# Performance work log

Hardware: AMD Instinct MI355X
Metric: run time of the kernel (lower is better)

## Reference

```python
import jax, jax.numpy as jnp
import numpy as np

B, S, D, K = 8, 1024, 1024, 8192


def setup_inputs() -> dict:
    key = jax.random.key(0)
    k1, k2 = jax.random.split(key)
    z = jax.random.normal(k1, (B, S, D), dtype=jnp.float32)
    codebook = jax.random.normal(k2, (K, D), dtype=jnp.float32)
    return {"z": z, "codebook": codebook}


def reference(z, codebook):
    # Eval-mode forward of VectorQuantizer (no EMA / dead-code side effects).
    b, s, d = z.shape
    z_flat = z.reshape(-1, d)                              # [N, D]
    # squared L2 distances: ||z||^2 + ||e||^2 - 2 z.e
    distances = (jnp.sum(z_flat * z_flat, axis=1, keepdims=True)
                 + jnp.sum(codebook * codebook, axis=1)
                 - 2.0 * jnp.einsum('nd,kd->nk', z_flat, codebook))  # [N, K]
    indices = jnp.argmin(distances, axis=1)                # [N]
    quantized = codebook[indices].reshape(b, s, d)         # gather
    loss = jnp.asarray(0.0, dtype=z.dtype)                 # eval mode
    # straight-through estimator
    quantized = z + jax.lax.stop_gradient(quantized - z)
    logits = -distances.reshape(b, s, -1)                  # [B, S, K]
    return quantized, indices.reshape(b, s), loss, logits
```

## Files before the change

kernel.cpp:

```cpp
#include <hip/hip_runtime.h>
#include <hip/hip_bf16.h>
#include <stdint.h>

#define NROWS 8192
#define KCODES 8192
#define DDIM 1024

#define Q_OFF    0
#define IDX_OFF  8388608
#define LOSS_OFF 8396800
#define LOG_OFF  8396801

using f32x4  = __attribute__((ext_vector_type(4))) float;
using s16x8  = __attribute__((ext_vector_type(8))) short;

__device__ __forceinline__ unsigned int forder(float f) {
  unsigned int u = __float_as_uint(f);
  return (u & 0x80000000u) ? ~u : (u | 0x80000000u);
}
__device__ __forceinline__ float finv(unsigned int u) {
  return (u & 0x80000000u) ? __uint_as_float(u & 0x7fffffffu) : __uint_as_float(~u);
}

__device__ __forceinline__ void gld_lds16(const void* g, void* l) {
  __builtin_amdgcn_global_load_lds((const __attribute__((address_space(1))) unsigned int*)g,
                                   (__attribute__((address_space(3))) unsigned int*)l,
                                   16, 0, 0);
}

__global__ __launch_bounds__(256) void vq_convert(const float* __restrict__ z,
                                                  const float* __restrict__ cb,
                                                  __hip_bfloat16* __restrict__ bfbuf,
                                                  float* __restrict__ nrm) {
  const int r = blockIdx.x;
  const float* src = (r < NROWS) ? (z + (size_t)r * DDIM)
                                 : (cb + (size_t)(r - NROWS) * DDIM);
  float4 v = reinterpret_cast<const float4*>(src)[threadIdx.x];
  float vv[4] = {v.x, v.y, v.z, v.w};
  ushort4 p;
  unsigned short us[4];
  #pragma unroll
  for (int j = 0; j < 4; ++j) {
    __hip_bfloat16 b = __float2bfloat16(vv[j]);
    __builtin_memcpy(&us[j], &b, 2);
  }
  p.x = us[0]; p.y = us[1]; p.z = us[2]; p.w = us[3];
  reinterpret_cast<ushort4*>(bfbuf + (size_t)r * DDIM)[threadIdx.x] = p;

  float s = vv[0]*vv[0] + vv[1]*vv[1] + vv[2]*vv[2] + vv[3]*vv[3];
  #pragma unroll
  for (int m = 32; m > 0; m >>= 1) s += __shfl_down(s, m, 64);
  __shared__ float red[4];
  if ((threadIdx.x & 63) == 0) red[threadIdx.x >> 6] = s;
  __syncthreads();
  if (threadIdx.x == 0) nrm[r] = red[0] + red[1] + red[2] + red[3];
}

__global__ __launch_bounds__(256, 3) void vq_mfma(const __hip_bfloat16* __restrict__ zb,
                                                  const __hip_bfloat16* __restrict__ cbb,
                                                  const float* __restrict__ nrm,
                                                  unsigned int* __restrict__ gmins,
                                                  float* __restrict__ out) {
  __shared__ s16x8 Asv[1024];
  __shared__ s16x8 Bsv[1024];

  const int wgid = blockIdx.x;
  const int stx = wgid & 7;
  const int idx = wgid >> 3;
  const int sty = idx >> 6;
  const int tt_ = idx & 63;
  const int bx = stx * 8 + (tt_ & 7);
  const int by = sty * 8 + (tt_ >> 3);

  const int k0 = bx * 128;
  const int n0 = by * 128;
  const int tid = threadIdx.x;
  const int wid = tid >> 6, lane = tid & 63;
  const int wm = wid >> 1, wn = wid & 1;
  const int l15 = lane & 15, l4 = lane >> 4;

  const int srow = lane >> 3;
  const int c    = lane & 7;
  const __hip_bfloat16* ga[4];
  const __hip_bfloat16* gb[4];
  int loff[4];
  #pragma unroll
  for (int q = 0; q < 4; ++q) {
    const int s = wid * 4 + q;
    const int row = s * 8 + srow;
    const int cg = c ^ (row & 7);
    ga[q] = zb  + (size_t)(n0 + row) * DDIM + cg * 8;
    gb[q] = cbb + (size_t)(k0 + row) * DDIM + cg * 8;
    loff[q] = s * 1024;
  }

  f32x4 acc[4][4];
  #pragma unroll
  for (int i = 0; i < 4; ++i)
    #pragma unroll
    for (int j = 0; j < 4; ++j) acc[i][j] = (f32x4){0.f, 0.f, 0.f, 0.f};

  for (int it = 0; it < 16; ++it) {
    const int d0 = it * 64;
    #pragma unroll
    for (int q = 0; q < 4; ++q) {
      gld_lds16(ga[q] + d0, (char*)Asv + loff[q]);
      gld_lds16(gb[q] + d0, (char*)Bsv + loff[q]);
    }
    __syncthreads();

    #pragma unroll
    for (int ks = 0; ks < 2; ++ks) {
      const int ch = ks * 4 + l4;
      s16x8 af[4], bf[4];
      #pragma unroll
      for (int f = 0; f < 4; ++f) {
        const int ar = wm * 64 + f * 16 + l15;
        af[f] = Asv[ar * 8 + (ch ^ (ar & 7))];
        const int br = wn * 64 + f * 16 + l15;
        bf[f] = Bsv[br * 8 + (ch ^ (br & 7))];
      }
      #pragma unroll
      for (int fm = 0; fm < 4; ++fm)
        #pragma unroll
        for (int fn = 0; fn < 4; ++fn)
          acc[fm][fn] = __builtin_amdgcn_mfma_f32_16x16x32_bf16(af[fm], bf[fn], acc[fm][fn], 0, 0, 0);
    }
    __syncthreads();
  }

  float ee[4];
  #pragma unroll
  for (int j = 0; j < 4; ++j) ee[j] = nrm[NROWS + k0 + wn * 64 + j * 16 + l15];

  float* logits = out + LOG_OFF;
  #pragma unroll
  for (int f = 0; f < 4; ++f) {
    #pragma unroll
    for (int r = 0; r < 4; ++r) {
      const int n = n0 + wm * 64 + f * 16 + l4 * 4 + r;
      const float zz = nrm[n];
      float rowmin = 3.4e38f;
      #pragma unroll
      for (int j = 0; j < 4; ++j) {
        const int k = k0 + wn * 64 + j * 16 + l15;
        const float dist = fmaf(-2.f, acc[f][j][r], zz + ee[j]);
        logits[(size_t)n * KCODES + k] = -dist;
        rowmin = fminf(rowmin, dist);
      }
      #pragma unroll
      for (int mm = 1; mm < 16; mm <<= 1)
        rowmin = fminf(rowmin, __shfl_xor(rowmin, mm, 64));
      if (l15 == 0) atomicMin(&gmins[(size_t)n * 32 + (bx >> 1)], forder(rowmin));
    }
  }
}

#define MARGIN 16.0f
__global__ __launch_bounds__(256) void vq_refine(const float* __restrict__ z,
                                                 const float* __restrict__ cb,
                                                 const float* __restrict__ nrm,
                                                 const unsigned int* __restrict__ gmins,
                                                 float* __restrict__ out) {
  const int n = blockIdx.x;
  const int tid = threadIdx.x;
  __shared__ float tminS[32];
  __shared__ float gminS;
  __shared__ int cnt;
  __shared__ int cand[64];
  __shared__ float red[4];

  if (tid < 32) tminS[tid] = finv(gmins[(size_t)n * 32 + tid]);
  if (tid == 0) cnt = 0;
  __syncthreads();
  if (tid == 0) {
    float g = tminS[0];
    #pragma unroll
    for (int i = 1; i < 32; ++i) g = fminf(g, tminS[i]);
    gminS = g;
  }
  __syncthreads();
  const float thr = gminS + MARGIN;

  const float* lrow = out + LOG_OFF + (size_t)n * KCODES;
  for (int g = 0; g < 32; ++g) {
    if (tminS[g] <= thr) {
      const float dist = -lrow[g * 256 + tid];
      if (dist <= thr) {
        const int p = atomicAdd(&cnt, 1);
        if (p < 64) cand[p] = g * 256 + tid;
      }
    }
  }
  __syncthreads();
  const int ncand = min(cnt, 64);

  const float zz = nrm[n];
  const float4 zv = reinterpret_cast<const float4*>(z + (size_t)n * DDIM)[tid];
  float bestd = 0.f;
  int bestk = -1;
  for (int ci = 0; ci < ncand; ++ci) {
    const int k = cand[ci];
    const float4 ev = reinterpret_cast<const float4*>(cb + (size_t)k * DDIM)[tid];
    float s = zv.x * ev.x + zv.y * ev.y + zv.z * ev.z + zv.w * ev.w;
    #pragma unroll
    for (int mm = 32; mm > 0; mm >>= 1) s += __shfl_down(s, mm, 64);
    if ((tid & 63) == 0) red[tid >> 6] = s;
    __syncthreads();
    const float dot = red[0] + red[1] + red[2] + red[3];
    const float dist = zz + nrm[NROWS + k] - 2.0f * dot;
    if (bestk < 0 || dist < bestd || (dist == bestd && k < bestk)) {
      bestd = dist; bestk = k;
    }
    __syncthreads();
  }

  const float4* src = reinterpret_cast<const float4*>(cb + (size_t)bestk * DDIM);
  float4* dst = reinterpret_cast<float4*>(out + (size_t)n * DDIM);
  dst[tid] = src[tid];
  if (tid == 0) {
    out[IDX_OFF + n] = (float)bestk;
    if (n == 0) out[LOSS_OFF] = 0.f;
  }
}

extern "C" void kernel_launch(void* const* d_in, const int* in_sizes, int n_in,
                              void* d_out, int out_size, void* d_ws, size_t ws_size,
                              hipStream_t stream) {
  const float* z  = (const float*)d_in[0];
  const float* cb = (const float*)d_in[1];
  float* out = (float*)d_out;

  float* nrm = (float*)d_ws;
  unsigned int* gmins = (unsigned int*)((char*)d_ws + 65536);

  __hip_bfloat16* bfbuf = (__hip_bfloat16*)out;
  const __hip_bfloat16* zbf  = bfbuf;
  const __hip_bfloat16* cbbf = bfbuf + (size_t)NROWS * DDIM;

  hipMemsetAsync((char*)d_ws + 65536, 0xFF, (size_t)NROWS * 32 * 4, stream);
  vq_convert<<<NROWS + KCODES, 256, 0, stream>>>(z, cb, bfbuf, nrm);
  vq_mfma<<<4096, 256, 0, stream>>>(zbf, cbbf, nrm, gmins, out);
  vq_refine<<<NROWS, 256, 0, stream>>>(z, cb, nrm, gmins, out);
}
```

Before: 231.4 us.

## Stage logits tile through LDS for aligned vectorized nontemporal stores

The logits region starts at an odd float offset, so scalar per-element stores are misaligned. The epilogue now writes each 128x128 distance tile into a swizzled LDS buffer shifted by one column. It then emits 16-byte-aligned nontemporal vector stores, with a few boundary columns written as scalars. It also hoists the row-norm loads and raises the launch-bounds occupancy hint from 3 to 4, which may add register pressure and extra barriers in the epilogue.

```diff
diff --git a/kernel.cpp b/kernel.cpp
--- a/kernel.cpp
+++ b/kernel.cpp
@@ -56,13 +56,14 @@
   if (threadIdx.x == 0) nrm[r] = red[0] + red[1] + red[2] + red[3];
 }
 
-__global__ __launch_bounds__(256, 3) void vq_mfma(const __hip_bfloat16* __restrict__ zb,
+__global__ __launch_bounds__(256, 4) void vq_mfma(const __hip_bfloat16* __restrict__ zb,
                                                   const __hip_bfloat16* __restrict__ cbb,
                                                   const float* __restrict__ nrm,
                                                   unsigned int* __restrict__ gmins,
                                                   float* __restrict__ out) {
-  __shared__ s16x8 Asv[1024];
-  __shared__ s16x8 Bsv[1024];
+  __shared__ s16x8 smem[2048];
+  s16x8* Asv = smem;
+  s16x8* Bsv = smem + 1024;
 
   const int wgid = blockIdx.x;
   const int stx = wgid & 7;
@@ -132,26 +133,71 @@
   float ee[4];
   #pragma unroll
   for (int j = 0; j < 4; ++j) ee[j] = nrm[NROWS + k0 + wn * 64 + j * 16 + l15];
+  float zzv[4][4];
+  #pragma unroll
+  for (int f = 0; f < 4; ++f)
+    #pragma unroll
+    for (int r = 0; r < 4; ++r)
+      zzv[f][r] = nrm[n0 + wm * 64 + f * 16 + l4 * 4 + r];
 
   float* logits = out + LOG_OFF;
+
   #pragma unroll
   for (int f = 0; f < 4; ++f) {
     #pragma unroll
     for (int r = 0; r < 4; ++r) {
       const int n = n0 + wm * 64 + f * 16 + l4 * 4 + r;
-      const float zz = nrm[n];
       float rowmin = 3.4e38f;
       #pragma unroll
       for (int j = 0; j < 4; ++j) {
-        const int k = k0 + wn * 64 + j * 16 + l15;
-        const float dist = fmaf(-2.f, acc[f][j][r], zz + ee[j]);
-        logits[(size_t)n * KCODES + k] = -dist;
+        const int col = wn * 64 + j * 16 + l15;
+        const float dist = fmaf(-2.f, acc[f][j][r], zzv[f][r] + ee[j]);
+        if ((j == 0 && wn == 0 && l15 < 3) || (j == 3 && wn == 1 && l15 == 15))
+          logits[(size_t)n * KCODES + k0 + col] = -dist;
         rowmin = fminf(rowmin, dist);
       }
       #pragma unroll
       for (int mm = 1; mm < 16; mm <<= 1)
         rowmin = fminf(rowmin, __shfl_xor(rowmin, mm, 64));
       if (l15 == 0) atomicMin(&gmins[(size_t)n * 32 + (bx >> 1)], forder(rowmin));
+    }
+  }
+
+  float* tb = (float*)smem;
+  #pragma unroll 1
+  for (int p = 0; p < 2; ++p) {
+    __syncthreads();
+    if (wm == p) {
+      #pragma unroll
+      for (int f = 0; f < 4; ++f) {
+        const int rowl_base = f * 16 + l4 * 4;
+        #pragma unroll
+        for (int r = 0; r < 4; ++r) {
+          const int rowl = rowl_base + r;
+          #pragma unroll
+          for (int j = 0; j < 4; ++j) {
+            const int col = wn * 64 + j * 16 + l15;
+            if (col < 127) {
+              const float dist = fmaf(-2.f, acc[f][j][r], zzv[f][r] + ee[j]);
+              const int cs = col + 1;
+              tb[rowl * 128 + (((cs >> 2) ^ (rowl & 31)) << 2) + (cs & 3)] = -dist;
+            }
+          }
+        }
+      }
+    }
+    __syncthreads();
+    const int row = tid & 63;
+    const int cg = tid >> 6;
+    const int n = n0 + p * 64 + row;
+    float* lb = out + (LOG_OFF - 1) + (size_t)n * KCODES + k0;
+    #pragma unroll
+    for (int m = 0; m < 8; ++m) {
+      const int cc = cg * 8 + m;
+      if (cc >= 1) {
+        f32x4 v = *reinterpret_cast<f32x4*>(tb + row * 128 + ((cc ^ (row & 31)) << 2));
+        __builtin_nontemporal_store(v, reinterpret_cast<f32x4*>(lb + 4 * cc));
+      }
     }
   }
 }
```

New measurement: 731.0 us. +215.9%, slower.

## Switch distance GEMM from bf16 to per-row scaled int8 MFMA

Applied to the files above, without the earlier changes.

Quantizes z and codebook rows to int8 with per-row absmax scales in the convert kernel and uses the i8 16x16x64 MFMA instruction, halving the K-loop iterations and the bytes staged through LDS. The epilogue rescales the int32 accumulators by both row scales to rebuild the fp32 distances. Occupancy hint is raised to 4 blocks per CU. This trades accuracy of the approximate logits for higher matrix throughput, and relies on the fp32 refine pass and its margin to recover exact argmin indices; the written logits become coarser approximations of the reference values.

```diff
diff --git a/kernel.cpp b/kernel.cpp
--- a/kernel.cpp
+++ b/kernel.cpp
@@ -12,7 +12,7 @@
 #define LOG_OFF  8396801
 
 using f32x4  = __attribute__((ext_vector_type(4))) float;
-using s16x8  = __attribute__((ext_vector_type(8))) short;
+using i32x4  = __attribute__((ext_vector_type(4))) int;
 
 __device__ __forceinline__ unsigned int forder(float f) {
   unsigned int u = __float_as_uint(f);
@@ -30,39 +30,55 @@
 
 __global__ __launch_bounds__(256) void vq_convert(const float* __restrict__ z,
                                                   const float* __restrict__ cb,
-                                                  __hip_bfloat16* __restrict__ bfbuf,
-                                                  float* __restrict__ nrm) {
+                                                  signed char* __restrict__ qbuf,
+                                                  float* __restrict__ nrm,
+                                                  float* __restrict__ scl) {
   const int r = blockIdx.x;
+  const int tid = threadIdx.x;
   const float* src = (r < NROWS) ? (z + (size_t)r * DDIM)
                                  : (cb + (size_t)(r - NROWS) * DDIM);
-  float4 v = reinterpret_cast<const float4*>(src)[threadIdx.x];
+  float4 v = reinterpret_cast<const float4*>(src)[tid];
   float vv[4] = {v.x, v.y, v.z, v.w};
-  ushort4 p;
-  unsigned short us[4];
+
+  float amax = fmaxf(fmaxf(fabsf(vv[0]), fabsf(vv[1])),
+                     fmaxf(fabsf(vv[2]), fabsf(vv[3])));
+  float ss = vv[0]*vv[0] + vv[1]*vv[1] + vv[2]*vv[2] + vv[3]*vv[3];
+  #pragma unroll
+  for (int m = 32; m > 0; m >>= 1) {
+    amax = fmaxf(amax, __shfl_down(amax, m, 64));
+    ss += __shfl_down(ss, m, 64);
+  }
+  __shared__ float rA[4], rS[4], sB;
+  if ((tid & 63) == 0) { rA[tid >> 6] = amax; rS[tid >> 6] = ss; }
+  __syncthreads();
+  if (tid == 0) {
+    const float a = fmaxf(fmaxf(rA[0], rA[1]), fmaxf(rA[2], rA[3]));
+    nrm[r] = rS[0] + rS[1] + rS[2] + rS[3];
+    const float s = fmaxf(a, 1e-20f) * (1.0f / 127.0f);
+    scl[r] = s;
+    sB = s;
+  }
+  __syncthreads();
+  const float inv = 1.0f / sB;
+  int q[4];
   #pragma unroll
   for (int j = 0; j < 4; ++j) {
-    __hip_bfloat16 b = __float2bfloat16(vv[j]);
-    __builtin_memcpy(&us[j], &b, 2);
-  }
-  p.x = us[0]; p.y = us[1]; p.z = us[2]; p.w = us[3];
-  reinterpret_cast<ushort4*>(bfbuf + (size_t)r * DDIM)[threadIdx.x] = p;
-
-  float s = vv[0]*vv[0] + vv[1]*vv[1] + vv[2]*vv[2] + vv[3]*vv[3];
-  #pragma unroll
-  for (int m = 32; m > 0; m >>= 1) s += __shfl_down(s, m, 64);
-  __shared__ float red[4];
-  if ((threadIdx.x & 63) == 0) red[threadIdx.x >> 6] = s;
-  __syncthreads();
-  if (threadIdx.x == 0) nrm[r] = red[0] + red[1] + red[2] + red[3];
-}
-
-__global__ __launch_bounds__(256, 3) void vq_mfma(const __hip_bfloat16* __restrict__ zb,
-                                                  const __hip_bfloat16* __restrict__ cbb,
+    int t = (int)rintf(vv[j] * inv);
+    q[j] = t < -127 ? -127 : (t > 127 ? 127 : t);
+  }
+  const int packed = (q[0] & 255) | ((q[1] & 255) << 8) |
+                     ((q[2] & 255) << 16) | (q[3] << 24);
+  reinterpret_cast<int*>(qbuf + (size_t)r * DDIM)[tid] = packed;
+}
+
+__global__ __launch_bounds__(256, 4) void vq_mfma(const signed char* __restrict__ zq,
+                                                  const signed char* __restrict__ cq,
                                                   const float* __restrict__ nrm,
+                                                  const float* __restrict__ scl,
                                                   unsigned int* __restrict__ gmins,
                                                   float* __restrict__ out) {
-  __shared__ s16x8 Asv[1024];
-  __shared__ s16x8 Bsv[1024];
+  __shared__ i32x4 Asv[1024];
+  __shared__ i32x4 Bsv[1024];
 
   const int wgid = blockIdx.x;
   const int stx = wgid & 7;
@@ -81,27 +97,27 @@
 
   const int srow = lane >> 3;
   const int c    = lane & 7;
-  const __hip_bfloat16* ga[4];
-  const __hip_bfloat16* gb[4];
+  const signed char* ga[4];
+  const signed char* gb[4];
   int loff[4];
   #pragma unroll
   for (int q = 0; q < 4; ++q) {
     const int s = wid * 4 + q;
     const int row = s * 8 + srow;
     const int cg = c ^ (row & 7);
-    ga[q] = zb  + (size_t)(n0 + row) * DDIM + cg * 8;
-    gb[q] = cbb + (size_t)(k0 + row) * DDIM + cg * 8;
+    ga[q] = zq + (size_t)(n0 + row) * DDIM + cg * 16;
+    gb[q] = cq + (size_t)(k0 + row) * DDIM + cg * 16;
     loff[q] = s * 1024;
   }
 
-  f32x4 acc[4][4];
+  i32x4 acc[4][4];
   #pragma unroll
   for (int i = 0; i < 4; ++i)
     #pragma unroll
-    for (int j = 0; j < 4; ++j) acc[i][j] = (f32x4){0.f, 0.f, 0.f, 0.f};
-
-  for (int it = 0; it < 16; ++it) {
-    const int d0 = it * 64;
+    for (int j = 0; j < 4; ++j) acc[i][j] = (i32x4){0, 0, 0, 0};
+
+  for (int it = 0; it < 8; ++it) {
+    const int d0 = it * 128;
     #pragma unroll
     for (int q = 0; q < 4; ++q) {
       gld_lds16(ga[q] + d0, (char*)Asv + loff[q]);
@@ -112,7 +128,7 @@
     #pragma unroll
     for (int ks = 0; ks < 2; ++ks) {
       const int ch = ks * 4 + l4;
-      s16x8 af[4], bf[4];
+      i32x4 af[4], bf[4];
       #pragma unroll
       for (int f = 0; f < 4; ++f) {
         const int ar = wm * 64 + f * 16 + l15;
@@ -124,14 +140,18 @@
       for (int fm = 0; fm < 4; ++fm)
         #pragma unroll
         for (int fn = 0; fn < 4; ++fn)
-          acc[fm][fn] = __builtin_amdgcn_mfma_f32_16x16x32_bf16(af[fm], bf[fn], acc[fm][fn], 0, 0, 0);
-    }
-    __syncthreads();
-  }
-
-  float ee[4];
-  #pragma unroll
-  for (int j = 0; j < 4; ++j) ee[j] = nrm[NROWS + k0 + wn * 64 + j * 16 + l15];
+          acc[fm][fn] = __builtin_amdgcn_mfma_i32_16x16x64_i8(af[fm], bf[fn], acc[fm][fn], 0, 0, 0);
+    }
+    __syncthreads();
+  }
+
+  float ee[4], sk[4];
+  #pragma unroll
+  for (int j = 0; j < 4; ++j) {
+    const int kk = k0 + wn * 64 + j * 16 + l15;
+    ee[j] = nrm[NROWS + kk];
+    sk[j] = scl[NROWS + kk];
+  }
 
   float* logits = out + LOG_OFF;
   #pragma unroll
@@ -140,11 +160,12 @@
     for (int r = 0; r < 4; ++r) {
       const int n = n0 + wm * 64 + f * 16 + l4 * 4 + r;
       const float zz = nrm[n];
+      const float sn2 = -2.0f * scl[n];
       float rowmin = 3.4e38f;
       #pragma unroll
       for (int j = 0; j < 4; ++j) {
         const int k = k0 + wn * 64 + j * 16 + l15;
-        const float dist = fmaf(-2.f, acc[f][j][r], zz + ee[j]);
+        const float dist = fmaf(sn2 * sk[j], (float)acc[f][j][r], zz + ee[j]);
         logits[(size_t)n * KCODES + k] = -dist;
         rowmin = fminf(rowmin, dist);
       }
@@ -232,14 +253,15 @@
   float* out = (float*)d_out;
 
   float* nrm = (float*)d_ws;
-  unsigned int* gmins = (unsigned int*)((char*)d_ws + 65536);
-
-  __hip_bfloat16* bfbuf = (__hip_bfloat16*)out;
-  const __hip_bfloat16* zbf  = bfbuf;
-  const __hip_bfloat16* cbbf = bfbuf + (size_t)NROWS * DDIM;
-
-  hipMemsetAsync((char*)d_ws + 65536, 0xFF, (size_t)NROWS * 32 * 4, stream);
-  vq_convert<<<NROWS + KCODES, 256, 0, stream>>>(z, cb, bfbuf, nrm);
-  vq_mfma<<<4096, 256, 0, stream>>>(zbf, cbbf, nrm, gmins, out);
+  float* scl = (float*)((char*)d_ws + 65536);
+  unsigned int* gmins = (unsigned int*)((char*)d_ws + 131072);
+
+  signed char* qbuf = (signed char*)out;
+  const signed char* zq = qbuf;
+  const signed char* cq = qbuf + (size_t)NROWS * DDIM;
+
+  hipMemsetAsync((char*)d_ws + 131072, 0xFF, (size_t)NROWS * 32 * 4, stream);
+  vq_convert<<<NROWS + KCODES, 256, 0, stream>>>(z, cb, qbuf, nrm, scl);
+  vq_mfma<<<4096, 256, 0, stream>>>(zq, cq, nrm, scl, gmins, out);
   vq_refine<<<NROWS, 256, 0, stream>>>(z, cb, nrm, gmins, out);
 }
```

Result: faster. 208.2 us (-10.0%).
